# Performance work log

Hardware: AMD Instinct MI355X
Metric: run time of the kernel (lower is better)

## Reference

```python
import jax, jax.numpy as jnp
import numpy as np

N_FEATURES = 128
N_QUBITS = 10
Q_DEPTH = 4
N_OUTPUTS = 1
BATCH = 32768


def _apply_1q(psi, U, w, n):
    """Apply a single-qubit gate on wire w. psi: [B, 2^n]; U: [2,2] or [B,2,2]."""
    B = psi.shape[0]
    left, right = 2 ** w, 2 ** (n - 1 - w)
    psi = psi.reshape(B, left, 2, right)
    if U.ndim == 2:
        psi = jnp.einsum('ij,bljr->blir', U, psi)
    else:
        psi = jnp.einsum('bij,bljr->blir', U, psi)
    return psi.reshape(B, -1)


def _apply_cnot(psi, c, t, n):
    """CNOT(control=c, target=t) on psi [B, 2^n] (wire 0 = most significant bit)."""
    B = psi.shape[0]
    psi = psi.reshape((B,) + (2,) * n)
    ax_c, ax_t = c + 1, t + 1
    psi0 = jnp.take(psi, 0, axis=ax_c)
    psi1 = jnp.take(psi, 1, axis=ax_c)
    ax_t2 = ax_t - 1 if ax_t > ax_c else ax_t  # target axis shifts after removing control axis
    psi1 = jnp.flip(psi1, axis=ax_t2)          # flip target bit where control == 1
    psi = jnp.stack([psi0, psi1], axis=ax_c)
    return psi.reshape(B, -1)


def _rx_batched(theta):
    """RX(theta) per sample. theta: [B] -> U: [B,2,2] complex64."""
    c = jnp.cos(0.5 * theta).astype(jnp.complex64)
    s = jnp.sin(0.5 * theta).astype(jnp.complex64)
    row0 = jnp.stack([c, -1j * s], axis=-1)
    row1 = jnp.stack([-1j * s, c], axis=-1)
    return jnp.stack([row0, row1], axis=-2)


def _rot(phi, theta, omega):
    """Pennylane Rot = RZ(omega) @ RY(theta) @ RZ(phi), scalar angles -> [2,2] complex64."""
    c = jnp.cos(0.5 * theta)
    s = jnp.sin(0.5 * theta)
    u00 = jnp.exp(-0.5j * (phi + omega)) * c
    u01 = -jnp.exp(0.5j * (phi - omega)) * s
    u10 = jnp.exp(-0.5j * (phi - omega)) * s
    u11 = jnp.exp(0.5j * (phi + omega)) * c
    return jnp.stack([jnp.stack([u00, u01]), jnp.stack([u10, u11])]).astype(jnp.complex64)


def _quantum_forward(angles, q_weights):
    """Batched statevector sim: AngleEmbedding(RX) + StronglyEntanglingLayers, PauliZ expvals."""
    B, n = angles.shape
    depth = q_weights.shape[0]
    D = 2 ** n
    psi = jnp.zeros((B, D), jnp.complex64).at[:, 0].set(1.0)
    # AngleEmbedding: RX(angles[:, w]) on each wire (per-sample angles)
    for w in range(n):
        psi = _apply_1q(psi, _rx_batched(angles[:, w]), w, n)
    # StronglyEntanglingLayers: Rot on each wire, then CNOT ring with range r
    for l in range(depth):
        for w in range(n):
            U = _rot(q_weights[l, w, 0], q_weights[l, w, 1], q_weights[l, w, 2])
            psi = _apply_1q(psi, U, w, n)
        r = (l % (n - 1)) + 1
        for w in range(n):
            psi = _apply_cnot(psi, w, (w + r) % n, n)
    probs = psi.real ** 2 + psi.imag ** 2  # [B, D]
    # <Z_i> = sum_k probs[:,k] * (+1 if bit_i(k)==0 else -1); wire 0 = MSB
    bits = (jnp.arange(D)[None, :] >> (n - 1 - jnp.arange(n))[:, None]) & 1  # [n, D]
    signs = (1.0 - 2.0 * bits).astype(jnp.float32)
    return probs @ signs.T  # [B, n]


def setup_inputs() -> dict:
    key = jax.random.key(0)
    ks = jax.random.split(key, 5)
    x = jax.random.normal(ks[0], (BATCH, N_FEATURES), jnp.float32)
    W_pre = jax.random.normal(ks[1], (N_QUBITS, N_FEATURES), jnp.float32) / np.sqrt(N_FEATURES).astype(np.float32)
    b_pre = jnp.zeros((N_QUBITS,), jnp.float32)
    q_weights = 0.01 * jax.random.normal(ks[2], (Q_DEPTH, N_QUBITS, 3), jnp.float32)
    W_post = jax.random.normal(ks[3], (N_OUTPUTS, N_QUBITS), jnp.float32) / np.sqrt(N_QUBITS).astype(np.float32)
    b_post = jnp.zeros((N_OUTPUTS,), jnp.float32)
    return {"x": x, "W_pre": W_pre, "b_pre": b_pre, "q_weights": q_weights, "W_post": W_post, "b_post": b_post}


def reference(x, W_pre, b_pre, q_weights, W_post, b_post):
    angles = jnp.tanh(x @ W_pre.T + b_pre)        # pre_net + tanh -> [B, n_qubits]
    q_out = _quantum_forward(angles, q_weights)   # PauliZ expectations [B, n_qubits]
    return jax.nn.sigmoid(q_out @ W_post.T + b_post)
```

## Files before the change

### kernel.cpp

```cpp
#include <hip/hip_runtime.h>
#include <math.h>

#define BATCH 32768

typedef unsigned int u32;

#if defined(__has_builtin)
#if __has_builtin(__builtin_amdgcn_permlane32_swap) && __has_builtin(__builtin_amdgcn_permlane16_swap)
#define USE_PERMLANE 1
#else
#define USE_PERMLANE 0
#endif
#if __has_builtin(__builtin_amdgcn_fdot2)
#define HAS_FDOT2 1
#else
#define HAS_FDOT2 0
#endif
#else
#define USE_PERMLANE 0
#define HAS_FDOT2 0
#endif

struct GateC { unsigned prt, sel; };
struct CircuitT { GateC g[4][10]; unsigned srow[10]; };

constexpr CircuitT make_circuit() {
  CircuitT C{};
  unsigned row[10], col[10];
  for (int b = 0; b < 10; ++b) { row[b] = 1u << b; col[b] = 1u << b; }
  for (int l = 0; l < 4; ++l) {
    for (int w = 0; w < 10; ++w) {
      C.g[l][w].prt = col[9 - w];
      C.g[l][w].sel = row[9 - w];
    }
    const int r = (l % 9) + 1;
    for (int w = 0; w < 10; ++w) {
      const int c = w, t = (w + r) % 10;
      const int bc = 9 - c, bt = 9 - t;
      row[bt] ^= row[bc];
      col[bc] ^= col[bt];
    }
  }
  for (int i = 0; i < 10; ++i) C.srow[i] = row[9 - i];
  return C;
}
constexpr CircuitT CIRC = make_circuit();

constexpr int ORD[4][10] = {
  {0,1,2,3,4,5,6,7,8,9},
  {0,6,1,7,2,8,3,4,9,5},
  {0,2,1,3,7,4,8,5,9,6},
  {0,3,1,2,4,5,6,7,8,9},
};

template<int CTRL>
__device__ __forceinline__ u32 dppu(u32 v) {
  return (u32)__builtin_amdgcn_update_dpp((int)v, (int)v, CTRL, 0xF, 0xF, false);
}

template<int LOW>
__device__ __forceinline__ u32 dpp_low(u32 v) {
  static_assert(LOW >= 0 && LOW <= 15, "bad mask");
  if constexpr (LOW == 0) return v;
  else if constexpr (LOW == 1) return dppu<0xB1>(v);
  else if constexpr (LOW == 2) return dppu<0x4E>(v);
  else if constexpr (LOW == 3) return dppu<0x1B>(v);
  else if constexpr (LOW == 7) return dppu<0x141>(v);
  else if constexpr (LOW == 15) return dppu<0x140>(v);
  else if constexpr (LOW >= 4 && LOW <= 6) return dpp_low<LOW ^ 7>(dppu<0x141>(v));
  else return dpp_low<LOW ^ 15>(dppu<0x140>(v));
}

constexpr int dpp_ops_low(int low) {
  if (low == 0) return 0;
  if (low == 1 || low == 2 || low == 3 || low == 7 || low == 15) return 1;
  if ((low >= 4 && low <= 6) || low == 8 || (low >= 12 && low <= 14)) return 2;
  return 3;
}
constexpr int chain_cost(int M) {
#if !USE_PERMLANE
  if (M & 48) return 99;
#endif
  return ((M & 32) ? 2 : 0) + ((M & 16) ? 2 : 0) + dpp_ops_low(M & 15);
}
constexpr bool use_ds_mask(int M) { return chain_cost(M) >= 2; }

#if USE_PERMLANE
__device__ __forceinline__ u32 xor16u(u32 v, int lane) {
  auto r = __builtin_amdgcn_permlane16_swap(v, v, false, false);
  return (lane & 16) ? r[0] : r[1];
}
__device__ __forceinline__ u32 xor32u(u32 v, int lane) {
  auto r = __builtin_amdgcn_permlane32_swap(v, v, false, false);
  return (lane & 32) ? r[0] : r[1];
}
#else
__device__ __forceinline__ u32 xor16u(u32 v, int lane) { return (u32)__shfl_xor((int)v, 16, 64); }
__device__ __forceinline__ u32 xor32u(u32 v, int lane) { return (u32)__shfl_xor((int)v, 32, 64); }
#endif

template<int M>
__device__ __forceinline__ u32 lshuf(u32 v, int lane, int bpa) {
  if constexpr (use_ds_mask(M)) {
    if constexpr ((M & 32) != 0) {
      return (u32)__builtin_amdgcn_ds_bpermute(bpa, (int)v);
    } else {
      return (u32)__builtin_amdgcn_ds_swizzle((int)v, 0x1F | (M << 10));
    }
  } else {
    u32 t = v;
    if constexpr ((M & 32) != 0) t = xor32u(t, lane);
    if constexpr ((M & 16) != 0) t = xor16u(t, lane);
    if constexpr ((M & 15) != 0) t = dpp_low<M & 15>(t);
    return t;
  }
}

template<int CTRL>
__device__ __forceinline__ float dppf(float v) {
  const int i = __float_as_int(v);
  return __int_as_float(__builtin_amdgcn_update_dpp(i, i, CTRL, 0xF, 0xF, false));
}
__device__ __forceinline__ float shflx(float v, int m) { return __shfl_xor(v, m, 64); }

__device__ __forceinline__ float wave_sum(float v, int lane) {
  v += dppf<0xB1>(v);
  v += dppf<0x4E>(v);
  v += dppf<0x141>(v);
  v += dppf<0x140>(v);
#if USE_PERMLANE
  { auto r = __builtin_amdgcn_permlane16_swap(__float_as_uint(v), __float_as_uint(v), false, false);
    v = __uint_as_float(r[0]) + __uint_as_float(r[1]); }
  { auto r = __builtin_amdgcn_permlane32_swap(__float_as_uint(v), __float_as_uint(v), false, false);
    v = __uint_as_float(r[0]) + __uint_as_float(r[1]); }
#else
  v += shflx(v, 16);
  v += shflx(v, 32);
#endif
  return v;
}

__device__ __forceinline__ u32 pk_mul_h(u32 a, u32 b) {
  u32 d; asm("v_pk_mul_f16 %0, %1, %2" : "=v"(d) : "v"(a), "v"(b)); return d;
}
__device__ __forceinline__ u32 pk_fma_h(u32 a, u32 b, u32 c) {
  u32 d; asm("v_pk_fma_f16 %0, %1, %2, %3" : "=v"(d) : "v"(a), "v"(b), "v"(c)); return d;
}
__device__ __forceinline__ u32 pk_fma_hsw(u32 a, u32 b, u32 c) {
  u32 d;
  asm("v_pk_fma_f16 %0, %1, %2, %3 op_sel:[1,0,0] op_sel_hi:[0,1,1]"
      : "=v"(d) : "v"(a), "v"(b), "v"(c));
  return d;
}

__device__ __forceinline__ u32 pk2(float lo, float hi) {
  auto h = __builtin_amdgcn_cvt_pkrtz(lo, hi);
  return __builtin_bit_cast(u32, h);
}

__device__ __forceinline__ u32 updh(u32 a, u32 q, const uint4 s) {
  u32 t = pk_mul_h(a, s.x);
  t = pk_fma_hsw(a, s.y, t);
  t = pk_fma_h(q, s.z, t);
  t = pk_fma_hsw(q, s.w, t);
  return t;
}

template<int L, int W>
__device__ __forceinline__ void gate(u32 a[16], const u32* __restrict__ Ush, int lane) {
  constexpr unsigned PRT = CIRC.g[L][W].prt;
  constexpr unsigned SEL = CIRC.g[L][W].sel;
  constexpr int PLm = (int)(PRT >> 4), PRm = (int)(PRT & 15u);
  constexpr int SLm = (int)(SEL >> 4), SRm = (int)(SEL & 15u);

  int hl = 0;
  if constexpr (SLm != 0) hl = __popc(lane & SLm) & 1;

  const u32* gb = Ush + (L * 10 + W - 10) * 8;
  const uint4 cA = *(const uint4*)(gb + (hl << 2));
  uint4 cB;
  if constexpr (SRm != 0) cB = *(const uint4*)(gb + ((hl ^ 1) << 2));
  else                    cB = cA;

  int bpa = 0;
  if constexpr (use_ds_mask(PLm) && (PLm & 32) != 0) bpa = (lane ^ PLm) << 2;

  if constexpr (PLm == 0) {
    constexpr int LB = PRm & (-PRm);
#pragma unroll
    for (int t0 = 0; t0 < 16; ++t0) {
      if (t0 & LB) continue;
      const int t1 = t0 ^ PRm;
      const uint4 s0 = (__builtin_popcount((unsigned)(t0 & SRm)) & 1) ? cB : cA;
      const uint4 s1 = (__builtin_popcount((unsigned)(t1 & SRm)) & 1) ? cB : cA;
      const u32 a0 = a[t0], a1 = a[t1];
      a[t0] = updh(a0, a1, s0);
      a[t1] = updh(a1, a0, s1);
    }
  } else {
    u32 q[16];
#pragma unroll
    for (int t = 0; t < 16; ++t)
      q[t] = lshuf<PLm>(a[t ^ PRm], lane, bpa);
#pragma unroll
    for (int t = 0; t < 16; ++t) {
      const uint4 s = (__builtin_popcount((unsigned)(t & SRm)) & 1) ? cB : cA;
      a[t] = updh(a[t], q[t], s);
    }
  }
}

template<int L, int K>
__device__ __forceinline__ void layer_from(u32 a[16], const u32* __restrict__ Ush, int lane) {
  if constexpr (K < 10) {
    gate<L, ORD[L][K]>(a, Ush, lane);
    layer_from<L, K + 1>(a, Ush, lane);
  }
}

__global__ __launch_bounds__(256, 4) void qnn_kernel(
    const float* __restrict__ x, const float* __restrict__ Wpre,
    const float* __restrict__ bpre, const float* __restrict__ qw,
    const float* __restrict__ Wpost, const float* __restrict__ bpost,
    float* __restrict__ out)
{
  __shared__ __align__(16) u32 Ush[320];
  __shared__ float gtab[16 * 64];

  const int tid = threadIdx.x;
  if (tid < 40) {
    const float phi = qw[tid * 3 + 0];
    const float th  = qw[tid * 3 + 1];
    const float om  = qw[tid * 3 + 2];
    const float c = cosf(0.5f * th), s_ = sinf(0.5f * th);
    const float A  = c;
    const float Br = -cosf(phi) * s_, Bi = -sinf(phi) * s_;
    const float Cr =  cosf(om)  * s_, Ci =  sinf(om)  * s_;
    const float Dr =  cosf(phi + om) * c, Di = sinf(phi + om) * c;
    if (tid < 10) {
      u32* q = &Ush[240 + tid * 8];
      q[0] = __float_as_uint(A);  q[1] = __float_as_uint(Br);
      q[2] = __float_as_uint(Bi); q[3] = __float_as_uint(Cr);
      q[4] = __float_as_uint(Ci); q[5] = __float_as_uint(Dr);
      q[6] = __float_as_uint(Di); q[7] = 0u;
    } else {
      u32* p = &Ush[(tid - 10) * 8];
      p[0] = pk2(A, A);   p[1] = pk2(0.f, 0.f);
      p[2] = pk2(Br, Br); p[3] = pk2(-Bi, Bi);
      p[4] = pk2(Dr, Dr); p[5] = pk2(-Di, Di);
      p[6] = pk2(Cr, Cr); p[7] = pk2(-Ci, Ci);
    }
  }
#pragma unroll
  for (int k = 0; k < 4; ++k) {
    const int idx = tid * 4 + k;
    const int t = idx >> 6;
    const int l6 = idx & 63;
    float g = 0.f;
#pragma unroll
    for (int i = 0; i < 10; ++i) {
      const int sl = (int)(CIRC.srow[i] >> 4);
      const int sr = (int)(CIRC.srow[i] & 15u);
      const int par = (__popc(l6 & sl) + __popc(t & sr)) & 1;
      const float wv = Wpost[i];
      g += par ? -wv : wv;
    }
    gtab[t * 64 + l6] = g;
  }
  __syncthreads();

  const int lane = tid & 63;
  const int b = blockIdx.x * 4 + (tid >> 6);

  const float* xrow = x + (size_t)b * 128;
  const float x0 = xrow[lane];
  const float x1 = xrow[lane + 64];
  float cw[10], sw[10];
#pragma unroll
  for (int w = 0; w < 10; ++w) {
    float p = fmaf(x0, Wpre[w * 128 + lane], x1 * Wpre[w * 128 + 64 + lane]);
    p = wave_sum(p, lane);
    const float e = __expf(2.f * (p + bpre[w]));
    const float ang = 1.f - 2.f * __builtin_amdgcn_rcpf(e + 1.f);
    const float h = 0.5f * ang;
    cw[w] = __cosf(h);
    sw[w] = __sinf(h);
  }

  float u0r[10], u0i[10], u1r[10], u1i[10];
#pragma unroll
  for (int w = 0; w < 10; ++w) {
    const u32* q = &Ush[240 + w * 8];
    const float A = __uint_as_float(q[0]), Br = __uint_as_float(q[1]);
    const float Bi = __uint_as_float(q[2]), Cr = __uint_as_float(q[3]);
    const float Ci = __uint_as_float(q[4]), Dr = __uint_as_float(q[5]);
    const float Di = __uint_as_float(q[6]);
    const float ch = cw[w], sh = sw[w];
    u0r[w] = fmaf(A, ch, Bi * sh);
    u0i[w] = -Br * sh;
    u1r[w] = fmaf(Cr, ch, Di * sh);
    u1i[w] = fmaf(Ci, ch, -Dr * sh);
  }

  float Lr, Li;
  {
    const int b0 = (lane >> 5) & 1;
    Lr = b0 ? u1r[0] : u0r[0];
    Li = b0 ? u1i[0] : u0i[0];
  }
#pragma unroll
  for (int w = 1; w < 6; ++w) {
    const int bb = (lane >> (5 - w)) & 1;
    const float arv = bb ? u1r[w] : u0r[w];
    const float aiv = bb ? u1i[w] : u0i[w];
    const float nr = fmaf(Lr, arv, -Li * aiv);
    const float ni = fmaf(Lr, aiv, Li * arv);
    Lr = nr; Li = ni;
  }

  float t4r[4], t4i[4], lsr[4], lsi[4];
#pragma unroll
  for (int aa = 0; aa < 2; ++aa) {
#pragma unroll
    for (int c2 = 0; c2 < 2; ++c2) {
      const int k = (aa << 1) | c2;
      const float ar6 = aa ? u1r[6] : u0r[6], ai6 = aa ? u1i[6] : u0i[6];
      const float ar7 = c2 ? u1r[7] : u0r[7], ai7 = c2 ? u1i[7] : u0i[7];
      t4r[k] = fmaf(ar6, ar7, -ai6 * ai7);
      t4i[k] = fmaf(ar6, ai7, ai6 * ar7);
      const float ar8 = aa ? u1r[8] : u0r[8], ai8 = aa ? u1i[8] : u0i[8];
      const float ar9 = c2 ? u1r[9] : u0r[9], ai9 = c2 ? u1i[9] : u0i[9];
      const float s4r = fmaf(ar8, ar9, -ai8 * ai9);
      const float s4i = fmaf(ar8, ai9, ai8 * ar9);
      lsr[k] = fmaf(s4r, Lr, -s4i * Li);
      lsi[k] = fmaf(s4r, Li, s4i * Lr);
    }
  }

  u32 a[16];
#pragma unroll
  for (int t = 0; t < 16; ++t) {
    const int hi4 = t >> 2, lo4 = t & 3;
    const float re = fmaf(t4r[hi4], lsr[lo4], -t4i[hi4] * lsi[lo4]);
    const float im = fmaf(t4r[hi4], lsi[lo4],  t4i[hi4] * lsr[lo4]);
    a[t] = pk2(re, im);
  }

  layer_from<1, 0>(a, Ush, lane);
  layer_from<2, 0>(a, Ush, lane);
  layer_from<3, 0>(a, Ush, lane);

  float acc = 0.f;
#pragma unroll
  for (int t = 0; t < 16; ++t) {
    const float g = gtab[t * 64 + lane];
    float p;
#if HAS_FDOT2
    typedef _Float16 h2 __attribute__((ext_vector_type(2)));
    const h2 ah = __builtin_bit_cast(h2, a[t]);
    p = __builtin_amdgcn_fdot2(ah, ah, 0.f, false);
#else
    union H2U { u32 u; _Float16 h[2]; } z;
    z.u = a[t];
    const float rr = (float)z.h[0];
    const float ii = (float)z.h[1];
    p = fmaf(rr, rr, ii * ii);
#endif
    acc = fmaf(p, g, acc);
  }
  acc = wave_sum(acc, lane);

  if (lane == 0) {
    const float z = acc + bpost[0];
    out[b] = __builtin_amdgcn_rcpf(1.f + __expf(-z));
  }
}

extern "C" void kernel_launch(void* const* d_in, const int* in_sizes, int n_in,
                              void* d_out, int out_size, void* d_ws, size_t ws_size,
                              hipStream_t stream) {
  const float* x     = (const float*)d_in[0];
  const float* Wpre  = (const float*)d_in[1];
  const float* bpre  = (const float*)d_in[2];
  const float* qw    = (const float*)d_in[3];
  const float* Wpost = (const float*)d_in[4];
  const float* bpost = (const float*)d_in[5];
  float* out = (float*)d_out;

  (void)in_sizes; (void)n_in; (void)out_size; (void)d_ws; (void)ws_size;

  qnn_kernel<<<BATCH / 4, 256, 0, stream>>>(x, Wpre, bpre, qw, Wpost, bpost, out);
}
```

Baseline: 167.0 us.

## Process two samples per wavefront with interleaved gate updates

Each wavefront now simulates two batch samples instead of one. Each half-wave computes the pre-net projection for its own sample, and the cos/sin values are exchanged across halves with a permlane32 swap. The two statevectors are then updated together in every gate, which halves the block count and spreads the per-block setup (gate table, gtab) over twice as many samples. This adds instruction-level parallelism in the shuffle and FMA chains, but doubles the state registers per thread, which may hurt occupancy under the 256x4 launch bounds.

Result: faster. 159.2 us (-4.7%).

```diff
diff --git a/kernel.cpp b/kernel.cpp
--- a/kernel.cpp
+++ b/kernel.cpp
@@ -140,6 +140,29 @@
   return v;
 }
 
+__device__ __forceinline__ float half_sum(float v) {
+  v += dppf<0xB1>(v);
+  v += dppf<0x4E>(v);
+  v += dppf<0x141>(v);
+  v += dppf<0x140>(v);
+#if USE_PERMLANE
+  { auto r = __builtin_amdgcn_permlane16_swap(__float_as_uint(v), __float_as_uint(v), false, false);
+    v = __uint_as_float(r[0]) + __uint_as_float(r[1]); }
+#else
+  v += shflx(v, 16);
+#endif
+  return v;
+}
+
+__device__ __forceinline__ float xswapf(float v, int lane) {
+#if USE_PERMLANE
+  auto r = __builtin_amdgcn_permlane32_swap(__float_as_uint(v), __float_as_uint(v), false, false);
+  return (lane & 32) ? __uint_as_float(r[0]) : __uint_as_float(r[1]);
+#else
+  return shflx(v, 32);
+#endif
+}
+
 __device__ __forceinline__ u32 pk_mul_h(u32 a, u32 b) {
   u32 d; asm("v_pk_mul_f16 %0, %1, %2" : "=v"(d) : "v"(a), "v"(b)); return d;
 }
@@ -152,12 +175,10 @@
       : "=v"(d) : "v"(a), "v"(b), "v"(c));
   return d;
 }
-
 __device__ __forceinline__ u32 pk2(float lo, float hi) {
   auto h = __builtin_amdgcn_cvt_pkrtz(lo, hi);
   return __builtin_bit_cast(u32, h);
 }
-
 __device__ __forceinline__ u32 updh(u32 a, u32 q, const uint4 s) {
   u32 t = pk_mul_h(a, s.x);
   t = pk_fma_hsw(a, s.y, t);
@@ -167,7 +188,8 @@
 }
 
 template<int L, int W>
-__device__ __forceinline__ void gate(u32 a[16], const u32* __restrict__ Ush, int lane) {
+__device__ __forceinline__ void gate2(u32 a0[16], u32 a1[16],
+                                      const u32* __restrict__ Ush, int lane) {
   constexpr unsigned PRT = CIRC.g[L][W].prt;
   constexpr unsigned SEL = CIRC.g[L][W].sel;
   constexpr int PLm = (int)(PRT >> 4), PRm = (int)(PRT & 15u);
@@ -193,28 +215,92 @@
       const int t1 = t0 ^ PRm;
       const uint4 s0 = (__builtin_popcount((unsigned)(t0 & SRm)) & 1) ? cB : cA;
       const uint4 s1 = (__builtin_popcount((unsigned)(t1 & SRm)) & 1) ? cB : cA;
-      const u32 a0 = a[t0], a1 = a[t1];
-      a[t0] = updh(a0, a1, s0);
-      a[t1] = updh(a1, a0, s1);
+      const u32 x0 = a0[t0], x1 = a0[t1];
+      a0[t0] = updh(x0, x1, s0);
+      a0[t1] = updh(x1, x0, s1);
+      const u32 y0 = a1[t0], y1 = a1[t1];
+      a1[t0] = updh(y0, y1, s0);
+      a1[t1] = updh(y1, y0, s1);
     }
   } else {
-    u32 q[16];
-#pragma unroll
-    for (int t = 0; t < 16; ++t)
-      q[t] = lshuf<PLm>(a[t ^ PRm], lane, bpa);
 #pragma unroll
     for (int t = 0; t < 16; ++t) {
       const uint4 s = (__builtin_popcount((unsigned)(t & SRm)) & 1) ? cB : cA;
-      a[t] = updh(a[t], q[t], s);
+      const u32 q0 = lshuf<PLm>(a0[t ^ PRm], lane, bpa);
+      const u32 q1 = lshuf<PLm>(a1[t ^ PRm], lane, bpa);
+      a0[t] = updh(a0[t], q0, s);
+      a1[t] = updh(a1[t], q1, s);
     }
   }
 }
 
 template<int L, int K>
-__device__ __forceinline__ void layer_from(u32 a[16], const u32* __restrict__ Ush, int lane) {
+__device__ __forceinline__ void layer2_from(u32 a0[16], u32 a1[16],
+                                            const u32* __restrict__ Ush, int lane) {
   if constexpr (K < 10) {
-    gate<L, ORD[L][K]>(a, Ush, lane);
-    layer_from<L, K + 1>(a, Ush, lane);
+    gate2<L, ORD[L][K]>(a0, a1, Ush, lane);
+    layer2_from<L, K + 1>(a0, a1, Ush, lane);
+  }
+}
+
+__device__ __forceinline__ void build_state(u32 a[16], const float cw[10], const float sw[10],
+                                            const u32* __restrict__ Ush, int lane) {
+  float u0r[10], u0i[10], u1r[10], u1i[10];
+#pragma unroll
+  for (int w = 0; w < 10; ++w) {
+    const u32* q = &Ush[240 + w * 8];
+    const float A = __uint_as_float(q[0]), Br = __uint_as_float(q[1]);
+    const float Bi = __uint_as_float(q[2]), Cr = __uint_as_float(q[3]);
+    const float Ci = __uint_as_float(q[4]), Dr = __uint_as_float(q[5]);
+    const float Di = __uint_as_float(q[6]);
+    const float ch = cw[w], sh = sw[w];
+    u0r[w] = fmaf(A, ch, Bi * sh);
+    u0i[w] = -Br * sh;
+    u1r[w] = fmaf(Cr, ch, Di * sh);
+    u1i[w] = fmaf(Ci, ch, -Dr * sh);
+  }
+
+  float Lr, Li;
+  {
+    const int b0 = (lane >> 5) & 1;
+    Lr = b0 ? u1r[0] : u0r[0];
+    Li = b0 ? u1i[0] : u0i[0];
+  }
+#pragma unroll
+  for (int w = 1; w < 6; ++w) {
+    const int bb = (lane >> (5 - w)) & 1;
+    const float arv = bb ? u1r[w] : u0r[w];
+    const float aiv = bb ? u1i[w] : u0i[w];
+    const float nr = fmaf(Lr, arv, -Li * aiv);
+    const float ni = fmaf(Lr, aiv, Li * arv);
+    Lr = nr; Li = ni;
+  }
+
+  float t4r[4], t4i[4], lsr[4], lsi[4];
+#pragma unroll
+  for (int aa = 0; aa < 2; ++aa) {
+#pragma unroll
+    for (int c2 = 0; c2 < 2; ++c2) {
+      const int k = (aa << 1) | c2;
+      const float ar6 = aa ? u1r[6] : u0r[6], ai6 = aa ? u1i[6] : u0i[6];
+      const float ar7 = c2 ? u1r[7] : u0r[7], ai7 = c2 ? u1i[7] : u0i[7];
+      t4r[k] = fmaf(ar6, ar7, -ai6 * ai7);
+      t4i[k] = fmaf(ar6, ai7, ai6 * ar7);
+      const float ar8 = aa ? u1r[8] : u0r[8], ai8 = aa ? u1i[8] : u0i[8];
+      const float ar9 = c2 ? u1r[9] : u0r[9], ai9 = c2 ? u1i[9] : u0i[9];
+      const float s4r = fmaf(ar8, ar9, -ai8 * ai9);
+      const float s4i = fmaf(ar8, ai9, ai8 * ar9);
+      lsr[k] = fmaf(s4r, Lr, -s4i * Li);
+      lsi[k] = fmaf(s4r, Li, s4i * Lr);
+    }
+  }
+
+#pragma unroll
+  for (int t = 0; t < 16; ++t) {
+    const int hi4 = t >> 2, lo4 = t & 3;
+    const float re = fmaf(t4r[hi4], lsr[lo4], -t4i[hi4] * lsi[lo4]);
+    const float im = fmaf(t4r[hi4], lsi[lo4],  t4i[hi4] * lsr[lo4]);
+    a[t] = pk2(re, im);
   }
 }
 
@@ -270,109 +356,71 @@
   __syncthreads();
 
   const int lane = tid & 63;
-  const int b = blockIdx.x * 4 + (tid >> 6);
-
-  const float* xrow = x + (size_t)b * 128;
-  const float x0 = xrow[lane];
-  const float x1 = xrow[lane + 64];
-  float cw[10], sw[10];
+  const int wid = tid >> 6;
+  const int half = lane >> 5;
+  const int hl5 = lane & 31;
+  const int b0 = blockIdx.x * 8 + wid * 2;
+
+  const float* xr = x + (size_t)(b0 + half) * 128;
+  float xv[4];
+#pragma unroll
+  for (int k = 0; k < 4; ++k) xv[k] = xr[hl5 + 32 * k];
+
+  float cw0[10], sw0[10], cw1[10], sw1[10];
 #pragma unroll
   for (int w = 0; w < 10; ++w) {
-    float p = fmaf(x0, Wpre[w * 128 + lane], x1 * Wpre[w * 128 + 64 + lane]);
-    p = wave_sum(p, lane);
+    float p = 0.f;
+#pragma unroll
+    for (int k = 0; k < 4; ++k)
+      p = fmaf(xv[k], Wpre[w * 128 + hl5 + 32 * k], p);
+    p = half_sum(p);
     const float e = __expf(2.f * (p + bpre[w]));
     const float ang = 1.f - 2.f * __builtin_amdgcn_rcpf(e + 1.f);
     const float h = 0.5f * ang;
-    cw[w] = __cosf(h);
-    sw[w] = __sinf(h);
-  }
-
-  float u0r[10], u0i[10], u1r[10], u1i[10];
-#pragma unroll
-  for (int w = 0; w < 10; ++w) {
-    const u32* q = &Ush[240 + w * 8];
-    const float A = __uint_as_float(q[0]), Br = __uint_as_float(q[1]);
-    const float Bi = __uint_as_float(q[2]), Cr = __uint_as_float(q[3]);
-    const float Ci = __uint_as_float(q[4]), Dr = __uint_as_float(q[5]);
-    const float Di = __uint_as_float(q[6]);
-    const float ch = cw[w], sh = sw[w];
-    u0r[w] = fmaf(A, ch, Bi * sh);
-    u0i[w] = -Br * sh;
-    u1r[w] = fmaf(Cr, ch, Di * sh);
-    u1i[w] = fmaf(Ci, ch, -Dr * sh);
-  }
-
-  float Lr, Li;
-  {
-    const int b0 = (lane >> 5) & 1;
-    Lr = b0 ? u1r[0] : u0r[0];
-    Li = b0 ? u1i[0] : u0i[0];
-  }
-#pragma unroll
-  for (int w = 1; w < 6; ++w) {
-    const int bb = (lane >> (5 - w)) & 1;
-    const float arv = bb ? u1r[w] : u0r[w];
-    const float aiv = bb ? u1i[w] : u0i[w];
-    const float nr = fmaf(Lr, arv, -Li * aiv);
-    const float ni = fmaf(Lr, aiv, Li * arv);
-    Lr = nr; Li = ni;
-  }
-
-  float t4r[4], t4i[4], lsr[4], lsi[4];
-#pragma unroll
-  for (int aa = 0; aa < 2; ++aa) {
-#pragma unroll
-    for (int c2 = 0; c2 < 2; ++c2) {
-      const int k = (aa << 1) | c2;
-      const float ar6 = aa ? u1r[6] : u0r[6], ai6 = aa ? u1i[6] : u0i[6];
-      const float ar7 = c2 ? u1r[7] : u0r[7], ai7 = c2 ? u1i[7] : u0i[7];
-      t4r[k] = fmaf(ar6, ar7, -ai6 * ai7);
-      t4i[k] = fmaf(ar6, ai7, ai6 * ar7);
-      const float ar8 = aa ? u1r[8] : u0r[8], ai8 = aa ? u1i[8] : u0i[8];
-      const float ar9 = c2 ? u1r[9] : u0r[9], ai9 = c2 ? u1i[9] : u0i[9];
-      const float s4r = fmaf(ar8, ar9, -ai8 * ai9);
-      const float s4i = fmaf(ar8, ai9, ai8 * ar9);
-      lsr[k] = fmaf(s4r, Lr, -s4i * Li);
-      lsi[k] = fmaf(s4r, Li, s4i * Lr);
-    }
-  }
-
-  u32 a[16];
-#pragma unroll
-  for (int t = 0; t < 16; ++t) {
-    const int hi4 = t >> 2, lo4 = t & 3;
-    const float re = fmaf(t4r[hi4], lsr[lo4], -t4i[hi4] * lsi[lo4]);
-    const float im = fmaf(t4r[hi4], lsi[lo4],  t4i[hi4] * lsr[lo4]);
-    a[t] = pk2(re, im);
-  }
-
-  layer_from<1, 0>(a, Ush, lane);
-  layer_from<2, 0>(a, Ush, lane);
-  layer_from<3, 0>(a, Ush, lane);
-
-  float acc = 0.f;
+    const float c_own = __cosf(h);
+    const float s_own = __sinf(h);
+    const float c_oth = xswapf(c_own, lane);
+    const float s_oth = xswapf(s_own, lane);
+    cw0[w] = half ? c_oth : c_own;
+    sw0[w] = half ? s_oth : s_own;
+    cw1[w] = half ? c_own : c_oth;
+    sw1[w] = half ? s_own : s_oth;
+  }
+
+  u32 a0[16], a1[16];
+  build_state(a0, cw0, sw0, Ush, lane);
+  build_state(a1, cw1, sw1, Ush, lane);
+
+  layer2_from<1, 0>(a0, a1, Ush, lane);
+  layer2_from<2, 0>(a0, a1, Ush, lane);
+  layer2_from<3, 0>(a0, a1, Ush, lane);
+
+  float acc0 = 0.f, acc1 = 0.f;
 #pragma unroll
   for (int t = 0; t < 16; ++t) {
     const float g = gtab[t * 64 + lane];
-    float p;
 #if HAS_FDOT2
     typedef _Float16 h2 __attribute__((ext_vector_type(2)));
-    const h2 ah = __builtin_bit_cast(h2, a[t]);
-    p = __builtin_amdgcn_fdot2(ah, ah, 0.f, false);
-#else
-    union H2U { u32 u; _Float16 h[2]; } z;
-    z.u = a[t];
-    const float rr = (float)z.h[0];
-    const float ii = (float)z.h[1];
-    p = fmaf(rr, rr, ii * ii);
-#endif
-    acc = fmaf(p, g, acc);
-  }
-  acc = wave_sum(acc, lane);
+    const h2 ah0 = __builtin_bit_cast(h2, a0[t]);
+    const h2 ah1 = __builtin_bit_cast(h2, a1[t]);
+    acc0 = fmaf(__builtin_amdgcn_fdot2(ah0, ah0, 0.f, false), g, acc0);
+    acc1 = fmaf(__builtin_amdgcn_fdot2(ah1, ah1, 0.f, false), g, acc1);
+#else
+    union H2U { u32 u; _Float16 h[2]; } z0, z1;
+    z0.u = a0[t]; z1.u = a1[t];
+    const float r0 = (float)z0.h[0], i0 = (float)z0.h[1];
+    const float r1 = (float)z1.h[0], i1 = (float)z1.h[1];
+    acc0 = fmaf(fmaf(r0, r0, i0 * i0), g, acc0);
+    acc1 = fmaf(fmaf(r1, r1, i1 * i1), g, acc1);
+#endif
+  }
+  acc0 = wave_sum(acc0, lane);
+  acc1 = wave_sum(acc1, lane);
 
   if (lane == 0) {
-    const float z = acc + bpost[0];
-    out[b] = __builtin_amdgcn_rcpf(1.f + __expf(-z));
+    const float bp = bpost[0];
+    out[b0]     = __builtin_amdgcn_rcpf(1.f + __expf(-(acc0 + bp)));
+    out[b0 + 1] = __builtin_amdgcn_rcpf(1.f + __expf(-(acc1 + bp)));
   }
 }
 
@@ -389,5 +437,5 @@
 
   (void)in_sizes; (void)n_in; (void)out_size; (void)d_ws; (void)ws_size;
 
-  qnn_kernel<<<BATCH / 4, 256, 0, stream>>>(x, Wpre, bpre, qw, Wpost, bpost, out);
-}
+  qnn_kernel<<<BATCH / 8, 256, 0, stream>>>(x, Wpre, bpre, qw, Wpost, bpost, out);
+}
```
